# Kernel optimization log

Hardware: AMD Instinct MI355X
Metric: run time of the kernel (lower is better)

## Reference

```python
import jax, jax.numpy as jnp
import numpy as np

N_NODES = 50000
N_EDGES = 1_600_000


def gcn_conv(x, W, b, src, dst, ew, n_nodes):
    """PyG GCNConv: out = D^{-1/2}(A+I)D^{-1/2} (x W) + b, deg from edge_weight,
    self-loop weight = 1. Self-loop term handled analytically (norm = dinv[i]^2)."""
    xW = x @ W                                            # [N, F_out]
    deg = jax.ops.segment_sum(ew, dst, num_segments=n_nodes) + 1.0  # +1 self-loop
    dinv = jnp.where(deg > 0, jax.lax.rsqrt(deg), 0.0)    # [N]
    norm = dinv[src] * ew * dinv[dst]                     # [E]
    agg = jax.ops.segment_sum(norm[:, None] * xW[src], dst, num_segments=n_nodes)
    return agg + (dinv * dinv)[:, None] * xW + b


def setup_inputs() -> dict:
    key = jax.random.key(0)
    ks = jax.random.split(key, 9)
    s = lambda fi, fo: 1.0 / np.sqrt(fi)
    return {
        "x": jax.random.normal(ks[0], (N_NODES, 128), dtype=jnp.float32),
        "edge_index": jax.random.randint(ks[1], (2, N_EDGES), 0, N_NODES, dtype=jnp.int64)
        if jax.config.jax_enable_x64 else jax.random.randint(ks[1], (2, N_EDGES), 0, N_NODES, dtype=jnp.int32),
        "edge_weight": jax.random.uniform(ks[2], (N_EDGES,), dtype=jnp.float32),
        "W1": jax.random.normal(ks[3], (128, 64), dtype=jnp.float32) * s(128, 64),
        "b1": jnp.zeros((64,), dtype=jnp.float32),
        "W2": jax.random.normal(ks[4], (64, 64), dtype=jnp.float32) * s(64, 64),
        "b2": jnp.zeros((64,), dtype=jnp.float32),
        "W3": jax.random.normal(ks[5], (64, 40), dtype=jnp.float32) * s(64, 40),
        "b3": jnp.zeros((40,), dtype=jnp.float32),
    }


def reference(x, edge_index, edge_weight, W1, b1, W2, b2, W3, b3):
    src, dst = edge_index[0], edge_index[1]
    n = x.shape[0]
    h = jax.nn.relu(gcn_conv(x, W1, b1, src, dst, edge_weight, n))
    h = jax.nn.relu(gcn_conv(h, W2, b2, src, dst, edge_weight, n))
    return gcn_conv(h, W3, b3, src, dst, edge_weight, n)
```

## Files before the change

### kernel.cpp

```cpp
#include <hip/hip_runtime.h>


#define TILE 4096
#define BCAP_MAX 9216

static __device__ __forceinline__ float4 f4zero() { return make_float4(0.f, 0.f, 0.f, 0.f); }

static __device__ __forceinline__ unsigned short f2bf_rne(float x) {
    unsigned u = __float_as_uint(x);
    u += 0x7FFFu + ((u >> 16) & 1u);
    return (unsigned short)(u >> 16);
}

__global__ __launch_bounds__(1024) void bin_scatter_kernel(
        const int* __restrict__ src, const int* __restrict__ dst,
        const float* __restrict__ ew, int* __restrict__ bin_cursor,
        int2* __restrict__ binned, int E, int bcap) {
    __shared__ int cnt[256];
    __shared__ int scan[256];
    __shared__ int gbase[256];
    __shared__ int2 sorted[TILE];
    __shared__ unsigned char binof[TILE];
    const int tid = threadIdx.x;
    const int e0 = blockIdx.x * TILE;

    if (tid < 256) cnt[tid] = 0;
    __syncthreads();

    int mypk[4]; float myew[4]; int mybin[4]; int myrank[4]; bool myok[4];
    #pragma unroll
    for (int j = 0; j < 4; ++j) {
        int e = e0 + j * 1024 + tid;
        myok[j] = (e < E);
        if (myok[j]) {
            int d = dst[e];
            int s = src[e];
            myew[j]   = ew[e];
            mybin[j]  = d >> 8;
            mypk[j]   = (s << 8) | (d & 255);
            myrank[j] = atomicAdd(&cnt[mybin[j]], 1);
        }
    }
    __syncthreads();
    if (tid < 256) scan[tid] = cnt[tid];
    __syncthreads();
    for (int off = 1; off < 256; off <<= 1) {
        int v = 0;
        if (tid < 256) { v = scan[tid]; if (tid >= off) v += scan[tid - off]; }
        __syncthreads();
        if (tid < 256) scan[tid] = v;
        __syncthreads();
    }
    if (tid < 256 && cnt[tid] > 0)
        gbase[tid] = atomicAdd(&bin_cursor[tid], cnt[tid]);
    __syncthreads();
    #pragma unroll
    for (int j = 0; j < 4; ++j) {
        if (myok[j]) {
            int b = mybin[j];
            int slot = (scan[b] - cnt[b]) + myrank[j];
            sorted[slot] = make_int2(mypk[j], __float_as_int(myew[j]));
            binof[slot]  = (unsigned char)b;
        }
    }
    __syncthreads();
    const int total = scan[255];
    for (int i = tid; i < total; i += 1024) {
        int b = binof[i];
        int pos = gbase[b] + (i - (scan[b] - cnt[b]));
        if (pos < bcap)
            binned[(size_t)b * bcap + pos] = sorted[i];
    }
}

__global__ __launch_bounds__(1024) void bin_group_kernel(
        int2* __restrict__ binned, const int* __restrict__ bin_cursor,
        int* __restrict__ row_start, int* __restrict__ row_cnt,
        float* __restrict__ dinv, int N, int bcap) {
    __shared__ int   cntl[256];
    __shared__ float degl[256];
    __shared__ int   scan[256];
    __shared__ int   run[256];
    __shared__ int2  sorted[BCAP_MAX];
    const int b = blockIdx.x;
    const int tid = threadIdx.x;
    int n = bin_cursor[b];
    if (n > bcap) n = bcap;
    if (tid < 256) { cntl[tid] = 0; degl[tid] = 0.f; }
    __syncthreads();

    int2* seg = binned + (size_t)b * bcap;
    for (int i = tid; i < n; i += 1024) {
        int2 v = seg[i];
        int dl = v.x & 255;
        atomicAdd(&cntl[dl], 1);
        atomicAdd(&degl[dl], __int_as_float(v.y));
    }
    __syncthreads();
    if (tid < 256) scan[tid] = cntl[tid];
    __syncthreads();
    for (int off = 1; off < 256; off <<= 1) {
        int v = 0;
        if (tid < 256) { v = scan[tid]; if (tid >= off) v += scan[tid - off]; }
        __syncthreads();
        if (tid < 256) scan[tid] = v;
        __syncthreads();
    }
    if (tid < 256) {
        int ex = scan[tid] - cntl[tid];
        int d = (b << 8) + tid;
        if (d < N) {
            row_start[d] = b * bcap + ex;
            row_cnt[d]   = cntl[tid];
            dinv[d]      = rsqrtf(degl[tid] + 1.0f);
        }
        run[tid] = ex;
    }
    __syncthreads();
    for (int i = tid; i < n; i += 1024) {
        int2 v = seg[i];
        int dl = v.x & 255;
        int r = atomicAdd(&run[dl], 1);
        sorted[r] = make_int2(v.x >> 8, v.y);
    }
    __syncthreads();
    for (int i = tid; i < n; i += 1024)
        seg[i] = sorted[i];
}

template <int K, int M>
__global__ __launch_bounds__(256) void gemm_kernel(const float* __restrict__ X,
        const float* __restrict__ W, const float* __restrict__ dinv,
        unsigned short* __restrict__ Y, int N) {
    constexpr int KP = K + 4;
    __shared__ float xs[64 * KP];
    __shared__ float ws[K * M];
    const int tid = threadIdx.x;
    const int row0 = blockIdx.x * 64;

    for (int i = tid * 4; i < K * M; i += 1024)
        *(float4*)&ws[i] = *(const float4*)&W[i];

    const int nrows = min(64, N - row0);
    for (int i = tid * 4; i < 64 * K; i += 1024) {
        int r = i / K, k = i % K;
        float4 v = f4zero();
        if (r < nrows) v = *(const float4*)&X[(size_t)(row0 + r) * K + k];
        *(float4*)&xs[r * KP + k] = v;
    }
    __syncthreads();

    const int ct = tid & 15, rt = tid >> 4;
    const bool cok = (ct * 4 < M);
    float acc[4][4] = {};
    for (int k = 0; k < K; ++k) {
        float a0 = xs[(rt +  0) * KP + k];
        float a1 = xs[(rt + 16) * KP + k];
        float a2 = xs[(rt + 32) * KP + k];
        float a3 = xs[(rt + 48) * KP + k];
        float4 bv = cok ? *(const float4*)&ws[k * M + ct * 4] : f4zero();
        acc[0][0] += a0 * bv.x; acc[0][1] += a0 * bv.y; acc[0][2] += a0 * bv.z; acc[0][3] += a0 * bv.w;
        acc[1][0] += a1 * bv.x; acc[1][1] += a1 * bv.y; acc[1][2] += a1 * bv.z; acc[1][3] += a1 * bv.w;
        acc[2][0] += a2 * bv.x; acc[2][1] += a2 * bv.y; acc[2][2] += a2 * bv.z; acc[2][3] += a2 * bv.w;
        acc[3][0] += a3 * bv.x; acc[3][1] += a3 * bv.y; acc[3][2] += a3 * bv.z; acc[3][3] += a3 * bv.w;
    }
    if (cok) {
        #pragma unroll
        for (int i = 0; i < 4; ++i) {
            int r = row0 + rt + 16 * i;
            if (r < N) {
                float dd = dinv[r];
                ushort4 o;
                o.x = f2bf_rne(acc[i][0] * dd); o.y = f2bf_rne(acc[i][1] * dd);
                o.z = f2bf_rne(acc[i][2] * dd); o.w = f2bf_rne(acc[i][3] * dd);
                *(ushort4*)&Y[(size_t)r * M + ct * 4] = o;
            }
        }
    }
}

template <int F, bool RELU>
__global__ __launch_bounds__(256) void agg_kernel(const unsigned short* __restrict__ xw,
        const int2* __restrict__ csr, const int* __restrict__ row_start,
        const int* __restrict__ row_cnt, const float* __restrict__ dinv,
        const float* __restrict__ bias, float* __restrict__ out, int N) {
    constexpr int Q = F / 2;
    int wid = (int)((blockIdx.x * blockDim.x + threadIdx.x) >> 6);
    int lane = threadIdx.x & 63;
    if (wid >= N) return;
    const int half = lane >> 5;
    const int q = lane & 31;
    const bool qok = (q < Q);
    const unsigned* xw32 = (const unsigned*)xw;
    const int2* row = csr + row_start[wid];
    int cnt = row_cnt[wid];
    float a0l = 0.f, a0h = 0.f, a1l = 0.f, a1h = 0.f;
    for (int base = 0; base < cnt; base += 64) {
        int m = min(cnt - base, 64);
        int2 ed = make_int2(0, 0);
        if (lane < m) ed = row[base + lane];
        int j = 0;
        for (; j + 4 <= m; j += 4) {
            int   sA = __shfl(ed.x, j + half);
            float wA = __int_as_float(__shfl(ed.y, j + half));
            int   sB = __shfl(ed.x, j + 2 + half);
            float wB = __int_as_float(__shfl(ed.y, j + 2 + half));
            unsigned dA = 0, dB = 0;
            if (qok) {
                dA = xw32[(size_t)sA * Q + q];
                dB = xw32[(size_t)sB * Q + q];
            }
            a0l = fmaf(wA, __uint_as_float(dA << 16), a0l);
            a0h = fmaf(wA, __uint_as_float(dA & 0xFFFF0000u), a0h);
            a1l = fmaf(wB, __uint_as_float(dB << 16), a1l);
            a1h = fmaf(wB, __uint_as_float(dB & 0xFFFF0000u), a1h);
        }
        for (; j + 2 <= m; j += 2) {
            int   sA = __shfl(ed.x, j + half);
            float wA = __int_as_float(__shfl(ed.y, j + half));
            unsigned dA = 0;
            if (qok) dA = xw32[(size_t)sA * Q + q];
            a0l = fmaf(wA, __uint_as_float(dA << 16), a0l);
            a0h = fmaf(wA, __uint_as_float(dA & 0xFFFF0000u), a0h);
        }
        if (j < m) {
            int   s = __builtin_amdgcn_readlane(ed.x, j);
            float w = __int_as_float(__builtin_amdgcn_readlane(ed.y, j));
            unsigned d = 0;
            if (qok && half == 0) d = xw32[(size_t)s * Q + q];
            if (half == 0) {
                a1l = fmaf(w, __uint_as_float(d << 16), a1l);
                a1h = fmaf(w, __uint_as_float(d & 0xFFFF0000u), a1h);
            }
        }
    }
    float al = a0l + a1l, ah = a0h + a1h;
    al += __shfl_xor(al, 32);
    ah += __shfl_xor(ah, 32);
    if (half == 0 && qok) {
        float dd = dinv[wid];
        unsigned ds = xw32[(size_t)wid * Q + q];
        float2 bv = *(const float2*)&bias[2 * q];
        float ol = dd * (al + __uint_as_float(ds << 16)) + bv.x;
        float oh = dd * (ah + __uint_as_float(ds & 0xFFFF0000u)) + bv.y;
        if (RELU) { ol = fmaxf(ol, 0.f); oh = fmaxf(oh, 0.f); }
        *(float2*)&out[(size_t)wid * F + 2 * q] = make_float2(ol, oh);
    }
}

static inline size_t ws_align(size_t x) { return (x + 255) & ~(size_t)255; }

extern "C" void kernel_launch(void* const* d_in, const int* in_sizes, int n_in,
                              void* d_out, int out_size, void* d_ws, size_t ws_size,
                              hipStream_t stream) {
    const float* x  = (const float*)d_in[0];
    const int*   ei = (const int*)d_in[1];
    const float* ew = (const float*)d_in[2];
    const float* W1 = (const float*)d_in[3];
    const float* b1 = (const float*)d_in[4];
    const float* W2 = (const float*)d_in[5];
    const float* b2 = (const float*)d_in[6];
    const float* W3 = (const float*)d_in[7];
    const float* b3 = (const float*)d_in[8];
    float* out = (float*)d_out;

    const int N = in_sizes[0] / 128;
    const int E = in_sizes[1] / 2;
    const int* src = ei;
    const int* dst = ei + E;
    const int nbins = (N + 255) >> 8;

    char* p = (char*)d_ws;
    size_t off = 0;
    auto alloc = [&](size_t bytes) -> char* {
        char* q = p + off;
        off = ws_align(off + bytes);
        return q;
    };
    int*   row_start  = (int*)  alloc((size_t)N * 4);
    int*   row_cnt    = (int*)  alloc((size_t)N * 4);
    float* dinv       = (float*)alloc((size_t)N * 4);
    int*   bin_cursor = (int*)  alloc((size_t)nbins * 4);
    unsigned short* xwbuf = (unsigned short*)alloc((size_t)N * 64 * 2);
    float* hbuf       = (float*)alloc((size_t)N * 64 * 4);
    size_t remain = (ws_size > off) ? (ws_size - off) : 0;
    int bcap = (int)(remain / ((size_t)nbins * 8));
    if (bcap > BCAP_MAX) bcap = BCAP_MAX;
    int2* binned = (int2*)alloc((size_t)nbins * (size_t)bcap * 8);

    hipMemsetAsync(bin_cursor, 0, (size_t)nbins * 4, stream);

    const int tb = (E + TILE - 1) / TILE;
    const int gb = (N + 63) / 64;
    const int ab = (N + 3) / 4;

    bin_scatter_kernel<<<tb, 1024, 0, stream>>>(src, dst, ew, bin_cursor, binned, E, bcap);
    bin_group_kernel<<<nbins, 1024, 0, stream>>>(binned, bin_cursor, row_start, row_cnt, dinv, N, bcap);

    gemm_kernel<128, 64><<<gb, 256, 0, stream>>>(x, W1, dinv, xwbuf, N);
    agg_kernel<64, true><<<ab, 256, 0, stream>>>(xwbuf, binned, row_start, row_cnt, dinv, b1, hbuf, N);
    gemm_kernel<64, 64><<<gb, 256, 0, stream>>>(hbuf, W2, dinv, xwbuf, N);
    agg_kernel<64, true><<<ab, 256, 0, stream>>>(xwbuf, binned, row_start, row_cnt, dinv, b2, hbuf, N);
    gemm_kernel<64, 40><<<gb, 256, 0, stream>>>(hbuf, W3, dinv, xwbuf, N);
    agg_kernel<40, false><<<ab, 256, 0, stream>>>(xwbuf, binned, row_start, row_cnt, dinv, b3, out, N);
}
```

Before: 291.0 us.

## Split each aggregation into two source-range passes for L2 locality

Result: slower. 321.4 us (+10.4%).

```diff
diff --git a/kernel.cpp b/kernel.cpp
--- a/kernel.cpp
+++ b/kernel.cpp
@@ -11,6 +11,8 @@
     u += 0x7FFFu + ((u >> 16) & 1u);
     return (unsigned short)(u >> 16);
 }
+static __device__ __forceinline__ float bflo(unsigned d) { return __uint_as_float(d << 16); }
+static __device__ __forceinline__ float bfhi(unsigned d) { return __uint_as_float(d & 0xFFFF0000u); }
 
 __global__ __launch_bounds__(1024) void bin_scatter_kernel(
         const int* __restrict__ src, const int* __restrict__ dst,
@@ -75,52 +77,55 @@
 
 __global__ __launch_bounds__(1024) void bin_group_kernel(
         int2* __restrict__ binned, const int* __restrict__ bin_cursor,
-        int* __restrict__ row_start, int* __restrict__ row_cnt,
-        float* __restrict__ dinv, int N, int bcap) {
-    __shared__ int   cntl[256];
+        int* __restrict__ row_start, int* __restrict__ row_cnts,
+        float* __restrict__ dinv, int N, int bcap, int HALF) {
+    __shared__ int   cntl[512];
     __shared__ float degl[256];
-    __shared__ int   scan[256];
-    __shared__ int   run[256];
+    __shared__ int   scan[512];
+    __shared__ int   run[512];
     __shared__ int2  sorted[BCAP_MAX];
     const int b = blockIdx.x;
     const int tid = threadIdx.x;
     int n = bin_cursor[b];
     if (n > bcap) n = bcap;
-    if (tid < 256) { cntl[tid] = 0; degl[tid] = 0.f; }
+    if (tid < 512) cntl[tid] = 0;
+    if (tid < 256) degl[tid] = 0.f;
     __syncthreads();
 
     int2* seg = binned + (size_t)b * bcap;
     for (int i = tid; i < n; i += 1024) {
         int2 v = seg[i];
         int dl = v.x & 255;
-        atomicAdd(&cntl[dl], 1);
+        int key = (dl << 1) | (((v.x >> 8) >= HALF) ? 1 : 0);
+        atomicAdd(&cntl[key], 1);
         atomicAdd(&degl[dl], __int_as_float(v.y));
     }
     __syncthreads();
-    if (tid < 256) scan[tid] = cntl[tid];
-    __syncthreads();
-    for (int off = 1; off < 256; off <<= 1) {
+    if (tid < 512) scan[tid] = cntl[tid];
+    __syncthreads();
+    for (int off = 1; off < 512; off <<= 1) {
         int v = 0;
-        if (tid < 256) { v = scan[tid]; if (tid >= off) v += scan[tid - off]; }
+        if (tid < 512) { v = scan[tid]; if (tid >= off) v += scan[tid - off]; }
         __syncthreads();
-        if (tid < 256) scan[tid] = v;
+        if (tid < 512) scan[tid] = v;
         __syncthreads();
     }
+    if (tid < 512) run[tid] = scan[tid] - cntl[tid];
     if (tid < 256) {
-        int ex = scan[tid] - cntl[tid];
         int d = (b << 8) + tid;
         if (d < N) {
-            row_start[d] = b * bcap + ex;
-            row_cnt[d]   = cntl[tid];
+            int ex0 = scan[2 * tid] - cntl[2 * tid];
+            row_start[d] = b * bcap + ex0;
+            row_cnts[d]  = cntl[2 * tid] | (cntl[2 * tid + 1] << 16);
             dinv[d]      = rsqrtf(degl[tid] + 1.0f);
         }
-        run[tid] = ex;
     }
     __syncthreads();
     for (int i = tid; i < n; i += 1024) {
         int2 v = seg[i];
         int dl = v.x & 255;
-        int r = atomicAdd(&run[dl], 1);
+        int key = (dl << 1) | (((v.x >> 8) >= HALF) ? 1 : 0);
+        int r = atomicAdd(&run[key], 1);
         sorted[r] = make_int2(v.x >> 8, v.y);
     }
     __syncthreads();
@@ -179,10 +184,65 @@
     }
 }
 
-template <int F, bool RELU>
+template <int F>
+static __device__ __forceinline__ void seg_accum(const unsigned* __restrict__ xw32,
+        const int2* __restrict__ row, int cnt, int lane, int half, int q,
+        bool qok, float* AL, float* AH) {
+    constexpr int Q = F / 2;
+    float a[4][2] = {};
+    for (int base = 0; base < cnt; base += 64) {
+        int m = min(cnt - base, 64);
+        int2 ed = make_int2(0, 0);
+        if (lane < m) ed = row[base + lane];
+        int j = 0;
+        for (; j + 8 <= m; j += 8) {
+            int   s0 = __shfl(ed.x, j     + half);
+            float w0 = __int_as_float(__shfl(ed.y, j     + half));
+            int   s1 = __shfl(ed.x, j + 2 + half);
+            float w1 = __int_as_float(__shfl(ed.y, j + 2 + half));
+            int   s2 = __shfl(ed.x, j + 4 + half);
+            float w2 = __int_as_float(__shfl(ed.y, j + 4 + half));
+            int   s3 = __shfl(ed.x, j + 6 + half);
+            float w3 = __int_as_float(__shfl(ed.y, j + 6 + half));
+            unsigned d0 = 0, d1 = 0, d2 = 0, d3 = 0;
+            if (qok) {
+                d0 = xw32[(size_t)s0 * Q + q];
+                d1 = xw32[(size_t)s1 * Q + q];
+                d2 = xw32[(size_t)s2 * Q + q];
+                d3 = xw32[(size_t)s3 * Q + q];
+            }
+            a[0][0] = fmaf(w0, bflo(d0), a[0][0]); a[0][1] = fmaf(w0, bfhi(d0), a[0][1]);
+            a[1][0] = fmaf(w1, bflo(d1), a[1][0]); a[1][1] = fmaf(w1, bfhi(d1), a[1][1]);
+            a[2][0] = fmaf(w2, bflo(d2), a[2][0]); a[2][1] = fmaf(w2, bfhi(d2), a[2][1]);
+            a[3][0] = fmaf(w3, bflo(d3), a[3][0]); a[3][1] = fmaf(w3, bfhi(d3), a[3][1]);
+        }
+        for (; j + 2 <= m; j += 2) {
+            int   s = __shfl(ed.x, j + half);
+            float w = __int_as_float(__shfl(ed.y, j + half));
+            unsigned d = 0;
+            if (qok) d = xw32[(size_t)s * Q + q];
+            a[0][0] = fmaf(w, bflo(d), a[0][0]);
+            a[0][1] = fmaf(w, bfhi(d), a[0][1]);
+        }
+        if (j < m) {
+            int   s = __builtin_amdgcn_readlane(ed.x, j);
+            float w = __int_as_float(__builtin_amdgcn_readlane(ed.y, j));
+            unsigned d = 0;
+            if (qok && half == 0) d = xw32[(size_t)s * Q + q];
+            if (half == 0) {
+                a[1][0] = fmaf(w, bflo(d), a[1][0]);
+                a[1][1] = fmaf(w, bfhi(d), a[1][1]);
+            }
+        }
+    }
+    *AL = (a[0][0] + a[1][0]) + (a[2][0] + a[3][0]);
+    *AH = (a[0][1] + a[1][1]) + (a[2][1] + a[3][1]);
+}
+
+template <int F, int SEG, bool RELU>
 __global__ __launch_bounds__(256) void agg_kernel(const unsigned short* __restrict__ xw,
         const int2* __restrict__ csr, const int* __restrict__ row_start,
-        const int* __restrict__ row_cnt, const float* __restrict__ dinv,
+        const int* __restrict__ row_cnts, const float* __restrict__ dinv,
         const float* __restrict__ bias, float* __restrict__ out, int N) {
     constexpr int Q = F / 2;
     int wid = (int)((blockIdx.x * blockDim.x + threadIdx.x) >> 6);
@@ -192,59 +252,30 @@
     const int q = lane & 31;
     const bool qok = (q < Q);
     const unsigned* xw32 = (const unsigned*)xw;
-    const int2* row = csr + row_start[wid];
-    int cnt = row_cnt[wid];
-    float a0l = 0.f, a0h = 0.f, a1l = 0.f, a1h = 0.f;
-    for (int base = 0; base < cnt; base += 64) {
-        int m = min(cnt - base, 64);
-        int2 ed = make_int2(0, 0);
-        if (lane < m) ed = row[base + lane];
-        int j = 0;
-        for (; j + 4 <= m; j += 4) {
-            int   sA = __shfl(ed.x, j + half);
-            float wA = __int_as_float(__shfl(ed.y, j + half));
-            int   sB = __shfl(ed.x, j + 2 + half);
-            float wB = __int_as_float(__shfl(ed.y, j + 2 + half));
-            unsigned dA = 0, dB = 0;
-            if (qok) {
-                dA = xw32[(size_t)sA * Q + q];
-                dB = xw32[(size_t)sB * Q + q];
-            }
-            a0l = fmaf(wA, __uint_as_float(dA << 16), a0l);
-            a0h = fmaf(wA, __uint_as_float(dA & 0xFFFF0000u), a0h);
-            a1l = fmaf(wB, __uint_as_float(dB << 16), a1l);
-            a1h = fmaf(wB, __uint_as_float(dB & 0xFFFF0000u), a1h);
-        }
-        for (; j + 2 <= m; j += 2) {
-            int   sA = __shfl(ed.x, j + half);
-            float wA = __int_as_float(__shfl(ed.y, j + half));
-            unsigned dA = 0;
-            if (qok) dA = xw32[(size_t)sA * Q + q];
-            a0l = fmaf(wA, __uint_as_float(dA << 16), a0l);
-            a0h = fmaf(wA, __uint_as_float(dA & 0xFFFF0000u), a0h);
-        }
-        if (j < m) {
-            int   s = __builtin_amdgcn_readlane(ed.x, j);
-            float w = __int_as_float(__builtin_amdgcn_readlane(ed.y, j));
-            unsigned d = 0;
-            if (qok && half == 0) d = xw32[(size_t)s * Q + q];
-            if (half == 0) {
-                a1l = fmaf(w, __uint_as_float(d << 16), a1l);
-                a1h = fmaf(w, __uint_as_float(d & 0xFFFF0000u), a1h);
-            }
-        }
-    }
-    float al = a0l + a1l, ah = a0h + a1h;
+    int pc = row_cnts[wid];
+    int c0 = pc & 0xFFFF, c1 = pc >> 16;
+    const int2* row = csr + row_start[wid] + (SEG ? c0 : 0);
+    int cnt = SEG ? c1 : c0;
+    float al, ah;
+    seg_accum<F>(xw32, row, cnt, lane, half, q, qok, &al, &ah);
     al += __shfl_xor(al, 32);
     ah += __shfl_xor(ah, 32);
     if (half == 0 && qok) {
         float dd = dinv[wid];
-        unsigned ds = xw32[(size_t)wid * Q + q];
-        float2 bv = *(const float2*)&bias[2 * q];
-        float ol = dd * (al + __uint_as_float(ds << 16)) + bv.x;
-        float oh = dd * (ah + __uint_as_float(ds & 0xFFFF0000u)) + bv.y;
-        if (RELU) { ol = fmaxf(ol, 0.f); oh = fmaxf(oh, 0.f); }
-        *(float2*)&out[(size_t)wid * F + 2 * q] = make_float2(ol, oh);
+        float* op = &out[(size_t)wid * F + 2 * q];
+        if (SEG == 0) {
+            unsigned ds = xw32[(size_t)wid * Q + q];
+            float2 bv = *(const float2*)&bias[2 * q];
+            float ol = dd * (al + bflo(ds)) + bv.x;
+            float oh = dd * (ah + bfhi(ds)) + bv.y;
+            *(float2*)op = make_float2(ol, oh);
+        } else {
+            float2 prev = *(const float2*)op;
+            float ol = prev.x + dd * al;
+            float oh = prev.y + dd * ah;
+            if (RELU) { ol = fmaxf(ol, 0.f); oh = fmaxf(oh, 0.f); }
+            *(float2*)op = make_float2(ol, oh);
+        }
     }
 }
 
@@ -266,6 +297,7 @@
 
     const int N = in_sizes[0] / 128;
     const int E = in_sizes[1] / 2;
+    const int HALF = N / 2;
     const int* src = ei;
     const int* dst = ei + E;
     const int nbins = (N + 255) >> 8;
@@ -278,7 +310,7 @@
         return q;
     };
     int*   row_start  = (int*)  alloc((size_t)N * 4);
-    int*   row_cnt    = (int*)  alloc((size_t)N * 4);
+    int*   row_cnts   = (int*)  alloc((size_t)N * 4);
     float* dinv       = (float*)alloc((size_t)N * 4);
     int*   bin_cursor = (int*)  alloc((size_t)nbins * 4);
     unsigned short* xwbuf = (unsigned short*)alloc((size_t)N * 64 * 2);
@@ -295,12 +327,15 @@
     const int ab = (N + 3) / 4;
 
     bin_scatter_kernel<<<tb, 1024, 0, stream>>>(src, dst, ew, bin_cursor, binned, E, bcap);
-    bin_group_kernel<<<nbins, 1024, 0, stream>>>(binned, bin_cursor, row_start, row_cnt, dinv, N, bcap);
+    bin_group_kernel<<<nbins, 1024, 0, stream>>>(binned, bin_cursor, row_start, row_cnts, dinv, N, bcap, HALF);
 
     gemm_kernel<128, 64><<<gb, 256, 0, stream>>>(x, W1, dinv, xwbuf, N);
-    agg_kernel<64, true><<<ab, 256, 0, stream>>>(xwbuf, binned, row_start, row_cnt, dinv, b1, hbuf, N);
+    agg_kernel<64, 0, false><<<ab, 256, 0, stream>>>(xwbuf, binned, row_start, row_cnts, dinv, b1, hbuf, N);
+    agg_kernel<64, 1, true ><<<ab, 256, 0, stream>>>(xwbuf, binned, row_start, row_cnts, dinv, b1, hbuf, N);
     gemm_kernel<64, 64><<<gb, 256, 0, stream>>>(hbuf, W2, dinv, xwbuf, N);
-    agg_kernel<64, true><<<ab, 256, 0, stream>>>(xwbuf, binned, row_start, row_cnt, dinv, b2, hbuf, N);
+    agg_kernel<64, 0, false><<<ab, 256, 0, stream>>>(xwbuf, binned, row_start, row_cnts, dinv, b2, hbuf, N);
+    agg_kernel<64, 1, true ><<<ab, 256, 0, stream>>>(xwbuf, binned, row_start, row_cnts, dinv, b2, hbuf, N);
     gemm_kernel<64, 40><<<gb, 256, 0, stream>>>(hbuf, W3, dinv, xwbuf, N);
-    agg_kernel<40, false><<<ab, 256, 0, stream>>>(xwbuf, binned, row_start, row_cnt, dinv, b3, out, N);
-}
+    agg_kernel<40, 0, false><<<ab, 256, 0, stream>>>(xwbuf, binned, row_start, row_cnts, dinv, b3, out, N);
+    agg_kernel<40, 1, false><<<ab, 256, 0, stream>>>(xwbuf, binned, row_start, row_cnts, dinv, b3, out, N);
+}
```

## Split 64-wide aggregation into two column-half passes with nontemporal CSR access

Applied to the files above, without the earlier changes.

Result: slower. 336.7 us (+15.7%).

```diff
diff --git a/kernel.cpp b/kernel.cpp
--- a/kernel.cpp
+++ b/kernel.cpp
@@ -11,6 +11,8 @@
     u += 0x7FFFu + ((u >> 16) & 1u);
     return (unsigned short)(u >> 16);
 }
+static __device__ __forceinline__ float bflo(unsigned d) { return __uint_as_float(d << 16); }
+static __device__ __forceinline__ float bfhi(unsigned d) { return __uint_as_float(d & 0xFFFF0000u); }
 
 __global__ __launch_bounds__(1024) void bin_scatter_kernel(
         const int* __restrict__ src, const int* __restrict__ dst,
@@ -179,59 +181,89 @@
     }
 }
 
-template <int F, bool RELU>
-__global__ __launch_bounds__(256) void agg_kernel(const unsigned short* __restrict__ xw,
+template <bool RELU>
+__global__ __launch_bounds__(256) void agg64_half_kernel(const unsigned* __restrict__ xw32,
+        const int2* __restrict__ csr, const int* __restrict__ row_start,
+        const int* __restrict__ row_cnt, const float* __restrict__ dinv,
+        const float* __restrict__ bias, float* __restrict__ out, int N, int qbase) {
+    int wid = (int)((blockIdx.x * blockDim.x + threadIdx.x) >> 6);
+    int lane = threadIdx.x & 63;
+    if (wid >= N) return;
+    const int quarter = lane >> 4;
+    const int q = lane & 15;
+    const unsigned long long* row =
+        (const unsigned long long*)(csr + row_start[wid]);
+    int cnt = row_cnt[wid];
+    float a0l = 0.f, a0h = 0.f, a1l = 0.f, a1h = 0.f;
+    for (int base = 0; base < cnt; base += 64) {
+        int m = min(cnt - base, 64);
+        int sx = 0, sy = 0;
+        if (lane < m) {
+            unsigned long long p = __builtin_nontemporal_load(row + base + lane);
+            sx = (int)p; sy = (int)(p >> 32);
+        }
+        for (int j = 0; j < m; j += 8) {
+            int   s0 = __shfl(sx, j + quarter);
+            float w0 = __int_as_float(__shfl(sy, j + quarter));
+            int   s1 = __shfl(sx, j + 4 + quarter);
+            float w1 = __int_as_float(__shfl(sy, j + 4 + quarter));
+            unsigned d0 = xw32[(size_t)s0 * 32 + qbase + q];
+            unsigned d1 = xw32[(size_t)s1 * 32 + qbase + q];
+            a0l = fmaf(w0, bflo(d0), a0l); a0h = fmaf(w0, bfhi(d0), a0h);
+            a1l = fmaf(w1, bflo(d1), a1l); a1h = fmaf(w1, bfhi(d1), a1h);
+        }
+    }
+    float al = a0l + a1l, ah = a0h + a1h;
+    al += __shfl_xor(al, 16); ah += __shfl_xor(ah, 16);
+    al += __shfl_xor(al, 32); ah += __shfl_xor(ah, 32);
+    if (lane < 16) {
+        float dd = dinv[wid];
+        unsigned ds = xw32[(size_t)wid * 32 + qbase + q];
+        int col = 2 * (qbase + q);
+        float ol = dd * (al + bflo(ds)) + bias[col];
+        float oh = dd * (ah + bfhi(ds)) + bias[col + 1];
+        if (RELU) { ol = fmaxf(ol, 0.f); oh = fmaxf(oh, 0.f); }
+        unsigned long long pk =
+            ((unsigned long long)__float_as_uint(oh) << 32) | __float_as_uint(ol);
+        __builtin_nontemporal_store(pk,
+            (unsigned long long*)&out[(size_t)wid * 64 + col]);
+    }
+}
+
+__global__ __launch_bounds__(256) void agg40_kernel(const unsigned* __restrict__ xw32,
         const int2* __restrict__ csr, const int* __restrict__ row_start,
         const int* __restrict__ row_cnt, const float* __restrict__ dinv,
         const float* __restrict__ bias, float* __restrict__ out, int N) {
-    constexpr int Q = F / 2;
+    constexpr int Q = 20;
     int wid = (int)((blockIdx.x * blockDim.x + threadIdx.x) >> 6);
     int lane = threadIdx.x & 63;
     if (wid >= N) return;
     const int half = lane >> 5;
     const int q = lane & 31;
     const bool qok = (q < Q);
-    const unsigned* xw32 = (const unsigned*)xw;
-    const int2* row = csr + row_start[wid];
+    const unsigned long long* row =
+        (const unsigned long long*)(csr + row_start[wid]);
     int cnt = row_cnt[wid];
     float a0l = 0.f, a0h = 0.f, a1l = 0.f, a1h = 0.f;
     for (int base = 0; base < cnt; base += 64) {
         int m = min(cnt - base, 64);
-        int2 ed = make_int2(0, 0);
-        if (lane < m) ed = row[base + lane];
-        int j = 0;
-        for (; j + 4 <= m; j += 4) {
-            int   sA = __shfl(ed.x, j + half);
-            float wA = __int_as_float(__shfl(ed.y, j + half));
-            int   sB = __shfl(ed.x, j + 2 + half);
-            float wB = __int_as_float(__shfl(ed.y, j + 2 + half));
-            unsigned dA = 0, dB = 0;
+        int sx = 0, sy = 0;
+        if (lane < m) {
+            unsigned long long p = __builtin_nontemporal_load(row + base + lane);
+            sx = (int)p; sy = (int)(p >> 32);
+        }
+        for (int j = 0; j < m; j += 4) {
+            int   s0 = __shfl(sx, j + half);
+            float w0 = __int_as_float(__shfl(sy, j + half));
+            int   s1 = __shfl(sx, j + 2 + half);
+            float w1 = __int_as_float(__shfl(sy, j + 2 + half));
+            unsigned d0 = 0, d1 = 0;
             if (qok) {
-                dA = xw32[(size_t)sA * Q + q];
-                dB = xw32[(size_t)sB * Q + q];
+                d0 = xw32[(size_t)s0 * Q + q];
+                d1 = xw32[(size_t)s1 * Q + q];
             }
-            a0l = fmaf(wA, __uint_as_float(dA << 16), a0l);
-            a0h = fmaf(wA, __uint_as_float(dA & 0xFFFF0000u), a0h);
-            a1l = fmaf(wB, __uint_as_float(dB << 16), a1l);
-            a1h = fmaf(wB, __uint_as_float(dB & 0xFFFF0000u), a1h);
-        }
-        for (; j + 2 <= m; j += 2) {
-            int   sA = __shfl(ed.x, j + half);
-            float wA = __int_as_float(__shfl(ed.y, j + half));
-            unsigned dA = 0;
-            if (qok) dA = xw32[(size_t)sA * Q + q];
-            a0l = fmaf(wA, __uint_as_float(dA << 16), a0l);
-            a0h = fmaf(wA, __uint_as_float(dA & 0xFFFF0000u), a0h);
-        }
-        if (j < m) {
-            int   s = __builtin_amdgcn_readlane(ed.x, j);
-            float w = __int_as_float(__builtin_amdgcn_readlane(ed.y, j));
-            unsigned d = 0;
-            if (qok && half == 0) d = xw32[(size_t)s * Q + q];
-            if (half == 0) {
-                a1l = fmaf(w, __uint_as_float(d << 16), a1l);
-                a1h = fmaf(w, __uint_as_float(d & 0xFFFF0000u), a1h);
-            }
+            a0l = fmaf(w0, bflo(d0), a0l); a0h = fmaf(w0, bfhi(d0), a0h);
+            a1l = fmaf(w1, bflo(d1), a1l); a1h = fmaf(w1, bfhi(d1), a1h);
         }
     }
     float al = a0l + a1l, ah = a0h + a1h;
@@ -240,11 +272,13 @@
     if (half == 0 && qok) {
         float dd = dinv[wid];
         unsigned ds = xw32[(size_t)wid * Q + q];
-        float2 bv = *(const float2*)&bias[2 * q];
-        float ol = dd * (al + __uint_as_float(ds << 16)) + bv.x;
-        float oh = dd * (ah + __uint_as_float(ds & 0xFFFF0000u)) + bv.y;
-        if (RELU) { ol = fmaxf(ol, 0.f); oh = fmaxf(oh, 0.f); }
-        *(float2*)&out[(size_t)wid * F + 2 * q] = make_float2(ol, oh);
+        int col = 2 * q;
+        float ol = dd * (al + bflo(ds)) + bias[col];
+        float oh = dd * (ah + bfhi(ds)) + bias[col + 1];
+        unsigned long long pk =
+            ((unsigned long long)__float_as_uint(oh) << 32) | __float_as_uint(ol);
+        __builtin_nontemporal_store(pk,
+            (unsigned long long*)&out[(size_t)wid * 40 + col]);
     }
 }
 
@@ -297,10 +331,14 @@
     bin_scatter_kernel<<<tb, 1024, 0, stream>>>(src, dst, ew, bin_cursor, binned, E, bcap);
     bin_group_kernel<<<nbins, 1024, 0, stream>>>(binned, bin_cursor, row_start, row_cnt, dinv, N, bcap);
 
+    const unsigned* xw32 = (const unsigned*)xwbuf;
+
     gemm_kernel<128, 64><<<gb, 256, 0, stream>>>(x, W1, dinv, xwbuf, N);
-    agg_kernel<64, true><<<ab, 256, 0, stream>>>(xwbuf, binned, row_start, row_cnt, dinv, b1, hbuf, N);
+    agg64_half_kernel<true ><<<ab, 256, 0, stream>>>(xw32, binned, row_start, row_cnt, dinv, b1, hbuf, N, 0);
+    agg64_half_kernel<true ><<<ab, 256, 0, stream>>>(xw32, binned, row_start, row_cnt, dinv, b1, hbuf, N, 16);
     gemm_kernel<64, 64><<<gb, 256, 0, stream>>>(hbuf, W2, dinv, xwbuf, N);
-    agg_kernel<64, true><<<ab, 256, 0, stream>>>(xwbuf, binned, row_start, row_cnt, dinv, b2, hbuf, N);
+    agg64_half_kernel<true ><<<ab, 256, 0, stream>>>(xw32, binned, row_start, row_cnt, dinv, b2, hbuf, N, 0);
+    agg64_half_kernel<true ><<<ab, 256, 0, stream>>>(xw32, binned, row_start, row_cnt, dinv, b2, hbuf, N, 16);
     gemm_kernel<64, 40><<<gb, 256, 0, stream>>>(hbuf, W3, dinv, xwbuf, N);
-    agg_kernel<40, false><<<ab, 256, 0, stream>>>(xwbuf, binned, row_start, row_cnt, dinv, b3, out, N);
-}
+    agg40_kernel<<<ab, 256, 0, stream>>>(xw32, binned, row_start, row_cnt, dinv, b3, out, N);
+}
```
